# Kernel optimization log

Hardware: AMD Instinct MI355X
Metric: run time of the kernel (lower is better)

Reference implementation:

```python
import jax, jax.numpy as jnp
import numpy as np

HIDDEN = 4096
INTER = 11008


def setup_inputs() -> dict:
    key = jax.random.key(0)
    k0, k1, k2, k3 = jax.random.split(key, 4)
    scale_h = 1.0 / np.sqrt(HIDDEN)
    scale_i = 1.0 / np.sqrt(INTER)
    return {
        "x": jax.random.normal(k0, (4, 32, HIDDEN), dtype=jnp.float32),
        "w_gate": jax.random.normal(k1, (INTER, HIDDEN), dtype=jnp.float32) * scale_h,
        "w_up": jax.random.normal(k2, (INTER, HIDDEN), dtype=jnp.float32) * scale_h,
        "w_down": jax.random.normal(k3, (HIDDEN, INTER), dtype=jnp.float32) * scale_i,
    }


def reference(x, w_gate, w_up, w_down):
    # SwiGLU MLP: down( silu(x @ Wg^T) * (x @ Wu^T) )
    gate = jax.nn.silu(jnp.einsum("bsh,ih->bsi", x, w_gate))
    up = jnp.einsum("bsh,ih->bsi", x, w_up)
    return jnp.einsum("bsi,hi->bsh", gate * up, w_down)
```

## Files before the change

### kernel.cpp

```cpp
#include <hip/hip_runtime.h>
#include <hip/hip_bf16.h>

#define HIDDEN 4096
#define INTER 11008
#define MTOK 128

typedef float f32x4 __attribute__((ext_vector_type(4)));
typedef short s16x8 __attribute__((ext_vector_type(8)));

__device__ __forceinline__ unsigned short f2bf(float f) {
    unsigned int u = __float_as_uint(f);
    u += 0x7FFFu + ((u >> 16) & 1u);
    return (unsigned short)(u >> 16);
}

__device__ __forceinline__ s16x8 cvt8(f32x4 a, f32x4 b) {
    s16x8 r;
    r[0] = (short)f2bf(a[0]); r[1] = (short)f2bf(a[1]);
    r[2] = (short)f2bf(a[2]); r[3] = (short)f2bf(a[3]);
    r[4] = (short)f2bf(b[0]); r[5] = (short)f2bf(b[1]);
    r[6] = (short)f2bf(b[2]); r[7] = (short)f2bf(b[3]);
    return r;
}

__global__ __launch_bounds__(256) void k_convert_x2(const float* __restrict__ x,
                                                    s16x8* __restrict__ xf) {
    int t = blockIdx.x * 256 + threadIdx.x;
    int lane = t & 63, kk2 = (t >> 6) & 1, mt = (t >> 7) & 7, s64 = t >> 10;
    int row = mt * 16 + (lane & 15);
    int k0 = s64 * 64 + kk2 * 32 + (lane >> 4) * 8;
    const float* p = x + (size_t)row * HIDDEN + k0;
    f32x4 a = *reinterpret_cast<const f32x4*>(p);
    f32x4 b = *reinterpret_cast<const f32x4*>(p + 4);
    xf[t] = cvt8(a, b);
}

__device__ __forceinline__ void loadA8(const s16x8* __restrict__ afb, int mt0, int s,
                                       int lane, s16x8 a[16]) {
#pragma unroll
    for (int kk = 0; kk < 8; ++kk)
#pragma unroll
        for (int mi = 0; mi < 2; ++mi) {
            int s64 = s * 4 + (kk >> 1), kk2 = kk & 1;
            a[kk * 2 + mi] = afb[(size_t)(((s64 * 8 + mt0 + mi) * 2 + kk2) * 64 + lane)];
        }
}

template <int LDK>
__device__ __forceinline__ void loadW16(const float* __restrict__ w, int row0,
                                        int lane, int s, f32x4 r[16]) {
    const float* base = w + (size_t)row0 * LDK + s * 256 + lane * 4;
#pragma unroll
    for (int j = 0; j < 16; ++j)
        r[j] = *reinterpret_cast<const f32x4*>(base + (size_t)j * LDK);
}

__device__ __forceinline__ void writeW16(char* wb, int wv, int lane, const f32x4 r[16]) {
#pragma unroll
    for (int j = 0; j < 16; ++j) {
        int row = wv * 16 + j;
        ushort4 o;
        o.x = f2bf(r[j][0]); o.y = f2bf(r[j][1]);
        o.z = f2bf(r[j][2]); o.w = f2bf(r[j][3]);
        *reinterpret_cast<ushort4*>(wb + row * 512 + ((lane * 8) ^ ((row & 7) << 4))) = o;
    }
}

__device__ __forceinline__ void comp8(const char* wb, int lane, const s16x8 a[16],
                                      f32x4 acc[2][4]) {
    const int r16 = lane & 15, g4 = lane >> 4;
#pragma unroll
    for (int nf = 0; nf < 4; ++nf) {
        int row = nf * 16 + r16;
        const char* wrp = wb + row * 512;
        unsigned swz = (unsigned)((row & 7) << 4);
#pragma unroll
        for (int kk = 0; kk < 8; ++kk) {
            s16x8 bf = *reinterpret_cast<const s16x8*>(wrp + ((unsigned)(kk * 64 + g4 * 16) ^ swz));
#pragma unroll
            for (int mi = 0; mi < 2; ++mi)
                acc[mi][nf] = __builtin_amdgcn_mfma_f32_16x16x32_bf16(a[kk * 2 + mi], bf,
                                                                      acc[mi][nf], 0, 0, 0);
        }
    }
}

template <int LDK>
__device__ __forceinline__ void gemm8(const s16x8* __restrict__ afb,
                                      const float* __restrict__ w, int n0,
                                      int sbeg, int send, f32x4 acc[2][4], char* wb) {
    const int tid = threadIdx.x, wv = tid >> 6, lane = tid & 63;
    const int mt0 = wv * 2;
    s16x8 a[16];
    f32x4 rw[16];

    loadW16<LDK>(w, n0 + wv * 16, lane, sbeg, rw);
    writeW16(wb, wv, lane, rw);
    __syncthreads();

    for (int s = sbeg; s < send; ++s) {
        const int buf = (s - sbeg) & 1;
        loadA8(afb, mt0, s, lane, a);
        __builtin_amdgcn_sched_barrier(0);
        if (s + 1 < send) loadW16<LDK>(w, n0 + wv * 16, lane, s + 1, rw);
        __builtin_amdgcn_sched_barrier(0);
        comp8(wb + buf * 32768, lane, a, acc);
        __builtin_amdgcn_sched_barrier(0);
        if (s + 1 < send) writeW16(wb + (buf ^ 1) * 32768, wv, lane, rw);
        __syncthreads();
    }
}

__global__ __launch_bounds__(256, 2) void k_gateup8(const s16x8* __restrict__ xf,
                                                    const float* __restrict__ wg,
                                                    const float* __restrict__ wu,
                                                    float* __restrict__ pg,
                                                    float* __restrict__ pu, int Sg) {
    __shared__ __align__(16) char wb[2 * 32768];
    const int gid = blockIdx.x;
    const int nt = gid % 172, rest = gid / 172;
    const int mat = rest & 1, kc = rest >> 1;
    const int n0 = nt * 64;
    const int nsteps = 16 / Sg;
    const int sbeg = kc * nsteps, send = sbeg + nsteps;

    f32x4 acc[2][4] = {};
    gemm8<HIDDEN>(xf, mat ? wu : wg, n0, sbeg, send, acc, wb);

    const int lane = threadIdx.x & 63, wv = threadIdx.x >> 6;
    const int r16 = lane & 15, g4 = lane >> 4;
    float* p = (mat ? pu : pg) + (size_t)kc * (MTOK * INTER);
#pragma unroll
    for (int mi = 0; mi < 2; ++mi)
#pragma unroll
        for (int nf = 0; nf < 4; ++nf)
#pragma unroll
            for (int r = 0; r < 4; ++r) {
                int m = (wv * 2 + mi) * 16 + g4 * 4 + r;
                p[(size_t)m * INTER + n0 + nf * 16 + r16] = acc[mi][nf][r];
            }
}

__global__ __launch_bounds__(256) void k_combine2(const float* __restrict__ pg,
                                                  const float* __restrict__ pu,
                                                  s16x8* __restrict__ hf, int Sg) {
    int t = blockIdx.x * 256 + threadIdx.x;
    int lane = t & 63, r16 = lane & 15, g4 = (lane >> 4) & 3;
    int kk2 = (t >> 6) & 1, mt = (t >> 7) & 7, s64 = t >> 10;
    int m = mt * 16 + r16;
    size_t base = (size_t)m * INTER + s64 * 64 + kk2 * 32 + g4 * 8;

    f32x4 g0 = (f32x4)0.0f, g1 = (f32x4)0.0f, u0 = (f32x4)0.0f, u1 = (f32x4)0.0f;
    for (int c = 0; c < Sg; ++c) {
        const float* pgc = pg + (size_t)c * (MTOK * INTER) + base;
        const float* puc = pu + (size_t)c * (MTOK * INTER) + base;
        g0 += *reinterpret_cast<const f32x4*>(pgc);
        g1 += *reinterpret_cast<const f32x4*>(pgc + 4);
        u0 += *reinterpret_cast<const f32x4*>(puc);
        u1 += *reinterpret_cast<const f32x4*>(puc + 4);
    }
    f32x4 h0, h1;
#pragma unroll
    for (int e = 0; e < 4; ++e) {
        h0[e] = g0[e] / (1.0f + __expf(-g0[e])) * u0[e];
        h1[e] = g1[e] / (1.0f + __expf(-g1[e])) * u1[e];
    }
    hf[t] = cvt8(h0, h1);
}

__global__ __launch_bounds__(256, 2) void k_down8(const s16x8* __restrict__ hf,
                                                  const float* __restrict__ wd,
                                                  float* __restrict__ pd, int Sd) {
    __shared__ __align__(16) char wb[2 * 32768];
    const int gid = blockIdx.x;
    const int nt = gid % 64, kc = gid / 64;
    const int n0 = nt * 64;
    const int sbeg = (43 * kc) / Sd, send = (43 * (kc + 1)) / Sd;

    f32x4 acc[2][4] = {};
    gemm8<INTER>(hf, wd, n0, sbeg, send, acc, wb);

    const int lane = threadIdx.x & 63, wv = threadIdx.x >> 6;
    const int r16 = lane & 15, g4 = lane >> 4;
    float* p = pd + (size_t)kc * (MTOK * HIDDEN);
#pragma unroll
    for (int mi = 0; mi < 2; ++mi)
#pragma unroll
        for (int nf = 0; nf < 4; ++nf)
#pragma unroll
            for (int r = 0; r < 4; ++r) {
                int m = (wv * 2 + mi) * 16 + g4 * 4 + r;
                p[(size_t)m * HIDDEN + n0 + nf * 16 + r16] = acc[mi][nf][r];
            }
}

__global__ __launch_bounds__(256) void k_reduce(const float* __restrict__ pd,
                                                float* __restrict__ out, int Sd) {
    int i = (blockIdx.x * 256 + threadIdx.x) * 4;
    const int NT = MTOK * HIDDEN;
    f32x4 s = (f32x4)0.0f;
    for (int c = 0; c < Sd; ++c)
        s += *reinterpret_cast<const f32x4*>(pd + (size_t)c * NT + i);
    *reinterpret_cast<f32x4*>(out + i) = s;
}

extern "C" void kernel_launch(void* const* d_in, const int* in_sizes, int n_in,
                              void* d_out, int out_size, void* d_ws, size_t ws_size,
                              hipStream_t stream) {
    const float* x  = (const float*)d_in[0];
    const float* wg = (const float*)d_in[1];
    const float* wu = (const float*)d_in[2];
    const float* wd = (const float*)d_in[3];
    float* out = (float*)d_out;

    const size_t XB = 1048576;
    const size_t HB = 2818048;
    const size_t PGU = (size_t)MTOK * INTER * 4;
    const size_t PD  = (size_t)MTOK * HIDDEN * 4;
    const int cfg[4][2] = {{2, 8}, {1, 4}, {1, 2}, {1, 1}};
    int Sg = 1, Sd = 1;
    for (int c = 0; c < 4; ++c) {
        size_t need = XB + HB + 2 * (size_t)cfg[c][0] * PGU + (size_t)cfg[c][1] * PD;
        if (need <= ws_size) { Sg = cfg[c][0]; Sd = cfg[c][1]; break; }
    }

    char* ws = (char*)d_ws;
    s16x8* xf = (s16x8*)ws;
    s16x8* hf = (s16x8*)(ws + XB);
    float* pg = (float*)(ws + XB + HB);
    float* pu = pg + (size_t)Sg * (MTOK * INTER);
    float* pd = pu + (size_t)Sg * (MTOK * INTER);

    k_convert_x2<<<256, 256, 0, stream>>>(x, xf);
    k_gateup8<<<172 * 2 * Sg, 256, 0, stream>>>(xf, wg, wu, pg, pu, Sg);
    k_combine2<<<688, 256, 0, stream>>>(pg, pu, hf, Sg);
    k_down8<<<64 * Sd, 256, 0, stream>>>(hf, wd, pd, Sd);
    k_reduce<<<512, 256, 0, stream>>>(pd, out, Sd);
}
```

Measured before the change: 152.2 us.

## Retile gate/up and down GEMMs to 32-wide N tiles with 1024-deep K stages

```diff
diff --git a/kernel.cpp b/kernel.cpp
--- a/kernel.cpp
+++ b/kernel.cpp
@@ -35,97 +35,94 @@
     xf[t] = cvt8(a, b);
 }
 
-__device__ __forceinline__ void loadA8(const s16x8* __restrict__ afb, int mt0, int s,
+__device__ __forceinline__ void loadA8(const s16x8* __restrict__ afb, int mt0, int s256,
                                        int lane, s16x8 a[16]) {
 #pragma unroll
     for (int kk = 0; kk < 8; ++kk)
 #pragma unroll
         for (int mi = 0; mi < 2; ++mi) {
-            int s64 = s * 4 + (kk >> 1), kk2 = kk & 1;
+            int s64 = s256 * 4 + (kk >> 1), kk2 = kk & 1;
             a[kk * 2 + mi] = afb[(size_t)(((s64 * 8 + mt0 + mi) * 2 + kk2) * 64 + lane)];
         }
 }
 
 template <int LDK>
-__device__ __forceinline__ void loadW16(const float* __restrict__ w, int row0,
-                                        int lane, int s, f32x4 r[16]) {
-    const float* base = w + (size_t)row0 * LDK + s * 256 + lane * 4;
-#pragma unroll
-    for (int j = 0; j < 16; ++j)
-        r[j] = *reinterpret_cast<const f32x4*>(base + (size_t)j * LDK);
-}
-
-__device__ __forceinline__ void writeW16(char* wb, int wv, int lane, const f32x4 r[16]) {
-#pragma unroll
-    for (int j = 0; j < 16; ++j) {
-        int row = wv * 16 + j;
-        ushort4 o;
-        o.x = f2bf(r[j][0]); o.y = f2bf(r[j][1]);
-        o.z = f2bf(r[j][2]); o.w = f2bf(r[j][3]);
-        *reinterpret_cast<ushort4*>(wb + row * 512 + ((lane * 8) ^ ((row & 7) << 4))) = o;
-    }
-}
-
-__device__ __forceinline__ void comp8(const char* wb, int lane, const s16x8 a[16],
-                                      f32x4 acc[2][4]) {
+__device__ __forceinline__ void gemm10(const s16x8* __restrict__ afb,
+                                       const float* __restrict__ w, int n0,
+                                       int sbeg, int nsteps, f32x4 acc[2][2],
+                                       char* wb) {
+    const int tid = threadIdx.x, wv = tid >> 6, lane = tid & 63;
     const int r16 = lane & 15, g4 = lane >> 4;
-#pragma unroll
-    for (int nf = 0; nf < 4; ++nf) {
-        int row = nf * 16 + r16;
-        const char* wrp = wb + row * 512;
-        unsigned swz = (unsigned)((row & 7) << 4);
-#pragma unroll
-        for (int kk = 0; kk < 8; ++kk) {
-            s16x8 bf = *reinterpret_cast<const s16x8*>(wrp + ((unsigned)(kk * 64 + g4 * 16) ^ swz));
-#pragma unroll
-            for (int mi = 0; mi < 2; ++mi)
-                acc[mi][nf] = __builtin_amdgcn_mfma_f32_16x16x32_bf16(a[kk * 2 + mi], bf,
-                                                                      acc[mi][nf], 0, 0, 0);
+
+    for (int t = 0; t < nsteps; ++t) {
+        const int s = sbeg + t;
+        const int kbase = s * 1024;
+        const int nq = (LDK == INTER && s == 10) ? 3 : 4;
+
+        f32x4 rw[8][4];
+#pragma unroll
+        for (int j = 0; j < 8; ++j) {
+            const float* rowp = w + (size_t)(n0 + wv * 8 + j) * LDK + kbase + lane * 4;
+#pragma unroll
+            for (int c = 0; c < 4; ++c)
+                if (c < nq) rw[j][c] = *reinterpret_cast<const f32x4*>(rowp + c * 256);
         }
-    }
-}
-
-template <int LDK>
-__device__ __forceinline__ void gemm8(const s16x8* __restrict__ afb,
-                                      const float* __restrict__ w, int n0,
-                                      int sbeg, int send, f32x4 acc[2][4], char* wb) {
-    const int tid = threadIdx.x, wv = tid >> 6, lane = tid & 63;
-    const int mt0 = wv * 2;
-    s16x8 a[16];
-    f32x4 rw[16];
-
-    loadW16<LDK>(w, n0 + wv * 16, lane, sbeg, rw);
-    writeW16(wb, wv, lane, rw);
-    __syncthreads();
-
-    for (int s = sbeg; s < send; ++s) {
-        const int buf = (s - sbeg) & 1;
-        loadA8(afb, mt0, s, lane, a);
-        __builtin_amdgcn_sched_barrier(0);
-        if (s + 1 < send) loadW16<LDK>(w, n0 + wv * 16, lane, s + 1, rw);
-        __builtin_amdgcn_sched_barrier(0);
-        comp8(wb + buf * 32768, lane, a, acc);
-        __builtin_amdgcn_sched_barrier(0);
-        if (s + 1 < send) writeW16(wb + (buf ^ 1) * 32768, wv, lane, rw);
+#pragma unroll
+        for (int j = 0; j < 8; ++j) {
+            const int row = wv * 8 + j;
+            const unsigned swz = (unsigned)((row & 7) << 4);
+            char* rowb = wb + row * 2048;
+#pragma unroll
+            for (int c = 0; c < 4; ++c)
+                if (c < nq) {
+                    ushort4 o;
+                    o.x = f2bf(rw[j][c][0]); o.y = f2bf(rw[j][c][1]);
+                    o.z = f2bf(rw[j][c][2]); o.w = f2bf(rw[j][c][3]);
+                    *reinterpret_cast<ushort4*>(rowb + ((unsigned)(c * 512 + lane * 8) ^ swz)) = o;
+                }
+        }
         __syncthreads();
-    }
-}
-
-__global__ __launch_bounds__(256, 2) void k_gateup8(const s16x8* __restrict__ xf,
-                                                    const float* __restrict__ wg,
-                                                    const float* __restrict__ wu,
-                                                    float* __restrict__ pg,
-                                                    float* __restrict__ pu, int Sg) {
-    __shared__ __align__(16) char wb[2 * 32768];
+
+#pragma unroll
+        for (int q = 0; q < 4; ++q)
+            if (q < nq) {
+                s16x8 a[16];
+                loadA8(afb, wv * 2, s * 4 + q, lane, a);
+#pragma unroll
+                for (int nf = 0; nf < 2; ++nf) {
+                    const int row = nf * 16 + r16;
+                    const char* rowb = wb + row * 2048;
+                    const unsigned swz = (unsigned)((row & 7) << 4);
+#pragma unroll
+                    for (int kk = 0; kk < 8; ++kk) {
+                        s16x8 bf = *reinterpret_cast<const s16x8*>(
+                            rowb + ((unsigned)(q * 512 + kk * 64 + g4 * 16) ^ swz));
+#pragma unroll
+                        for (int mi = 0; mi < 2; ++mi)
+                            acc[mi][nf] = __builtin_amdgcn_mfma_f32_16x16x32_bf16(
+                                a[kk * 2 + mi], bf, acc[mi][nf], 0, 0, 0);
+                    }
+                }
+            }
+        __syncthreads();
+    }
+}
+
+__global__ __launch_bounds__(256, 2) void k_gateup10(const s16x8* __restrict__ xf,
+                                                     const float* __restrict__ wg,
+                                                     const float* __restrict__ wu,
+                                                     float* __restrict__ pg,
+                                                     float* __restrict__ pu, int Sg) {
+    __shared__ __align__(16) char wb[32 * 2048];
     const int gid = blockIdx.x;
-    const int nt = gid % 172, rest = gid / 172;
+    const int nt = gid % 344, rest = gid / 344;
     const int mat = rest & 1, kc = rest >> 1;
-    const int n0 = nt * 64;
-    const int nsteps = 16 / Sg;
-    const int sbeg = kc * nsteps, send = sbeg + nsteps;
-
-    f32x4 acc[2][4] = {};
-    gemm8<HIDDEN>(xf, mat ? wu : wg, n0, sbeg, send, acc, wb);
+    const int n0 = nt * 32;
+    const int nsteps = 4 / Sg;
+    const int sbeg = kc * nsteps;
+
+    f32x4 acc[2][2] = {};
+    gemm10<HIDDEN>(xf, mat ? wu : wg, n0, sbeg, nsteps, acc, wb);
 
     const int lane = threadIdx.x & 63, wv = threadIdx.x >> 6;
     const int r16 = lane & 15, g4 = lane >> 4;
@@ -133,7 +130,7 @@
 #pragma unroll
     for (int mi = 0; mi < 2; ++mi)
 #pragma unroll
-        for (int nf = 0; nf < 4; ++nf)
+        for (int nf = 0; nf < 2; ++nf)
 #pragma unroll
             for (int r = 0; r < 4; ++r) {
                 int m = (wv * 2 + mi) * 16 + g4 * 4 + r;
@@ -168,17 +165,17 @@
     hf[t] = cvt8(h0, h1);
 }
 
-__global__ __launch_bounds__(256, 2) void k_down8(const s16x8* __restrict__ hf,
-                                                  const float* __restrict__ wd,
-                                                  float* __restrict__ pd, int Sd) {
-    __shared__ __align__(16) char wb[2 * 32768];
+__global__ __launch_bounds__(256, 2) void k_down10(const s16x8* __restrict__ hf,
+                                                   const float* __restrict__ wd,
+                                                   float* __restrict__ pd, int Sd) {
+    __shared__ __align__(16) char wb[32 * 2048];
     const int gid = blockIdx.x;
-    const int nt = gid % 64, kc = gid / 64;
-    const int n0 = nt * 64;
-    const int sbeg = (43 * kc) / Sd, send = (43 * (kc + 1)) / Sd;
-
-    f32x4 acc[2][4] = {};
-    gemm8<INTER>(hf, wd, n0, sbeg, send, acc, wb);
+    const int nt = gid % 128, kc = gid / 128;
+    const int n0 = nt * 32;
+    const int sbeg = (11 * kc) / Sd, send = (11 * (kc + 1)) / Sd;
+
+    f32x4 acc[2][2] = {};
+    gemm10<INTER>(hf, wd, n0, sbeg, send - sbeg, acc, wb);
 
     const int lane = threadIdx.x & 63, wv = threadIdx.x >> 6;
     const int r16 = lane & 15, g4 = lane >> 4;
@@ -186,7 +183,7 @@
 #pragma unroll
     for (int mi = 0; mi < 2; ++mi)
 #pragma unroll
-        for (int nf = 0; nf < 4; ++nf)
+        for (int nf = 0; nf < 2; ++nf)
 #pragma unroll
             for (int r = 0; r < 4; ++r) {
                 int m = (wv * 2 + mi) * 16 + g4 * 4 + r;
@@ -217,7 +214,7 @@
     const size_t HB = 2818048;
     const size_t PGU = (size_t)MTOK * INTER * 4;
     const size_t PD  = (size_t)MTOK * HIDDEN * 4;
-    const int cfg[4][2] = {{2, 8}, {1, 4}, {1, 2}, {1, 1}};
+    const int cfg[4][2] = {{2, 4}, {1, 4}, {1, 2}, {1, 1}};
     int Sg = 1, Sd = 1;
     for (int c = 0; c < 4; ++c) {
         size_t need = XB + HB + 2 * (size_t)cfg[c][0] * PGU + (size_t)cfg[c][1] * PD;
@@ -232,8 +229,8 @@
     float* pd = pu + (size_t)Sg * (MTOK * INTER);
 
     k_convert_x2<<<256, 256, 0, stream>>>(x, xf);
-    k_gateup8<<<172 * 2 * Sg, 256, 0, stream>>>(xf, wg, wu, pg, pu, Sg);
+    k_gateup10<<<344 * 2 * Sg, 256, 0, stream>>>(xf, wg, wu, pg, pu, Sg);
     k_combine2<<<688, 256, 0, stream>>>(pg, pu, hf, Sg);
-    k_down8<<<64 * Sd, 256, 0, stream>>>(hf, wd, pd, Sd);
+    k_down10<<<128 * Sd, 256, 0, stream>>>(hf, wd, pd, Sd);
     k_reduce<<<512, 256, 0, stream>>>(pd, out, Sd);
 }
```

After: 229.3 us. 50.6% more time.
